# Performance work log

Measured on AMD Instinct MI355X. Metric: run time of the kernel, lower is better.

## Reference

```python
import math
import jax, jax.numpy as jnp
import numpy as np

EPS = 1e-5  # BatchNorm1d default eps


def setup_inputs() -> dict:
    key = jax.random.key(0)
    ks = jax.random.split(key, 8)
    B, H, N, L, CD = 16, 64, 64, 16384, 3
    dt_min, dt_max = 1e-3, 1e-1
    # DSSM parameters (as in __init__)
    log_dt = jax.random.uniform(ks[0], (H,)) * (math.log(dt_max) - math.log(dt_min)) + math.log(dt_min)
    C_ri = jax.random.normal(ks[1], (H, N, 2))  # view_as_real of complex C
    log_A_real = jnp.log(0.5 * jnp.ones((H, N)))
    A_imag = math.pi * jnp.tile(jnp.arange(N, dtype=jnp.float32)[None, :], (H, 1))
    D = jax.random.normal(ks[2], (H,))
    # FiLM adaptor: Linear(cond_dim, 2*H)
    film_w = jax.random.normal(ks[3], (2 * H, CD)) / np.sqrt(CD)
    film_b = jnp.zeros((2 * H,))
    u = jax.random.normal(ks[4], (B, H, L))
    cond = jax.random.uniform(ks[5], (B, CD))
    length = jax.random.randint(ks[6], (B,), 1, L + 1)
    return dict(u=u, cond=cond, length=length, log_dt=log_dt, C_ri=C_ri,
                log_A_real=log_A_real, A_imag=A_imag, D=D,
                film_w=film_w, film_b=film_b)


def _dssm(u, length, log_dt, C_ri, log_A_real, A_imag, D):
    # u: (B, H, L). Length-agnostic equivalent of the torch length-bucketed path:
    # mask input beyond each example's length (bucket slicing u[idxs,:,:l]),
    # do one full-length linear FFT conv, then zero output beyond the length
    # (out[idxs,:,:l] = y leaves the tail at zero).
    B, H, L = u.shape
    dt = jnp.exp(log_dt)                       # (H,)
    C = C_ri[..., 0] + 1j * C_ri[..., 1]       # (H, N) complex
    A = -jnp.exp(log_A_real) + 1j * A_imag     # (H, N) complex
    dtA = A * dt[:, None]                      # (H, N)
    t = jnp.arange(L, dtype=jnp.float32)
    P = jnp.exp(dtA[:, :, None] * t)           # (H, N, L) complex
    Ck = C * (jnp.exp(dtA) - 1.0) / A          # (H, N)
    K = 2.0 * jnp.einsum('hn,hnl->hl', Ck, P).real  # (H, L) real kernel
    mask = (t[None, :] < length[:, None]).astype(u.dtype)  # (B, L)
    um = u * mask[:, None, :]
    n = 2 * L  # rfft size; linear conv of length-L signals has length 2L-1 <= 2L
    y = jnp.fft.irfft(jnp.fft.rfft(um, n=n) * jnp.fft.rfft(K, n=n)[None], n=n)[..., :L]
    y = (y + um * D[:, None]) * mask[:, None, :]
    return y


def _film(y, cond, film_w, film_b):
    # BatchNorm1d(affine=False), training-mode batch stats over (B, L) per channel
    H = y.shape[1]
    gb = cond @ film_w.T + film_b               # (B, 2H)
    g, b = gb[:, :H, None], gb[:, H:, None]
    mean = y.mean(axis=(0, 2))
    var = y.var(axis=(0, 2))                    # biased variance (torch BN normalization)
    yn = (y - mean[None, :, None]) * jax.lax.rsqrt(var[None, :, None] + EPS)
    return yn * g + b


def reference(u, cond, length, log_dt, C_ri, log_A_real, A_imag, D, film_w, film_b):
    y = _dssm(u, length, log_dt, C_ri, log_A_real, A_imag, D)
    y = _film(y, cond, film_w, film_b)
    y = jnp.tanh(y)
    return u + y  # residual connection around the conditioned SSM block
```

## Files before the change

### kernel.cpp

```cpp
#include <hip/hip_runtime.h>
#include <hip/hip_bf16.h>

typedef __hip_bfloat16 bf16;
typedef __attribute__((ext_vector_type(8))) short s16x8;
typedef __attribute__((ext_vector_type(4))) float f32x4;

#define SWZ(c) ((((c) ^ ((c) >> 3)) & 7) << 4)

__device__ __forceinline__ unsigned short f2b(float x){
    __hip_bfloat16 h = __float2bfloat16(x);
    return __builtin_bit_cast(unsigned short, h);
}
__device__ __forceinline__ float b2f(unsigned short s){
    unsigned int u = (unsigned int)s << 16;
    return __builtin_bit_cast(float, u);
}

__global__ __launch_bounds__(256) void k0_setup(const float* __restrict__ log_dt,
        const float* __restrict__ C_ri, const float* __restrict__ log_A_real,
        const float* __restrict__ A_imag, const float* __restrict__ Dp,
        float* __restrict__ rLtab, float* __restrict__ rStab,
        short* __restrict__ Qh,
        short* __restrict__ Pmh, short* __restrict__ Pml,
        short* __restrict__ Klh, short* __restrict__ Kll)
{
    __shared__ float arr[64][65];
    __shared__ float a0[64];
    __shared__ float kd[64];
    int h = blockIdx.x;
    int tid = threadIdx.x;
    int n = tid & 63, g = tid >> 6;
    int hn = h * 64 + n;
    double dtd  = exp((double)log_dt[h]);
    float  Aref = -expf(log_A_real[hn]);
    double Ared = (double)Aref;
    double Aimd = (double)A_imag[hn];
    double adt  = Aimd * dtd;
    float  mdt  = (float)(Ared * dtd);
    auto cexp = [&](float e, float& re, float& im){
        double a = adt * (double)e;
        double k = floor(a * 0.15915494309189535);
        float ang = (float)(a - k * 6.283185307179586);
        float si, co;
        __sincosf(ang, &si, &co);
        float mag = expf(mdt * e);
        re = mag * co; im = mag * si;
    };
    float rre, rim; cexp(1.f, rre, rim);
    float Cre = C_ri[2 * hn], Cim = C_ri[2 * hn + 1];
    float emre = rre - 1.f, emim = rim;
    float inva2 = 1.f / (Aref * Aref + (float)(Aimd * Aimd));
    float qre_ = (emre * Aref + emim * (float)Aimd) * inva2;
    float qim_ = (emim * Aref - emre * (float)Aimd) * inva2;
    float ckre = Cre * qre_ - Cim * qim_;
    float ckim = Cre * qim_ + Cim * qre_;
    {
        short* q0 = Qh + (size_t)h * 8192 + (2 * n) * 64;
        short* q1 = q0 + 64;
        for (int t = 16 * g; t < 16 * g + 16; ++t) {
            float pre, pim; cexp((float)(63 - t), pre, pim);
            q0[t] = (short)f2b(pre);
            q1[t] = (short)f2b(pim);
        }
    }
    if (g == 0) {
        float pre, pim; cexp(64.f, pre, pim);
        rLtab[2 * hn] = pre; rLtab[2 * hn + 1] = pim;
    }
    if (g == 1) {
        float pre, pim; cexp(1024.f, pre, pim);
        rStab[2 * hn] = pre; rStab[2 * hn + 1] = pim;
    }
    if (g == 2) a0[n] = 2.f * ckre;
    {
        short* pmh = Pmh + (size_t)h * 8192;
        short* pml = Pml + (size_t)h * 8192;
        for (int j = 16 * g; j < 16 * g + 16; ++j) {
            float pre, pim; cexp((float)(j + 1), pre, pim);
            float wre = 2.f * (ckre * pre - ckim * pim);
            float wim = 2.f * (ckre * pim + ckim * pre);
            unsigned short h0 = f2b(wre), h1 = f2b(-wim);
            pmh[j * 128 + 2 * n]     = (short)h0;
            pml[j * 128 + 2 * n]     = (short)f2b(wre - b2f(h0));
            pmh[j * 128 + 2 * n + 1] = (short)h1;
            pml[j * 128 + 2 * n + 1] = (short)f2b(-wim - b2f(h1));
            arr[j][n] = wre;
        }
    }
    __syncthreads();
    if (tid < 64) {
        int d = tid;
        float s = 0.f;
        if (d == 0) { for (int k = 0; k < 64; ++k) s += a0[k]; }
        else        { for (int k = 0; k < 64; ++k) s += arr[d - 1][k]; }
        kd[d] = s;
    }
    __syncthreads();
    {
        float Dh = Dp[h];
        short* klh = Klh + (size_t)h * 4096 + n * 64;
        short* kll = Kll + (size_t)h * 4096 + n * 64;
        for (int t = 16 * g; t < 16 * g + 16; ++t) {
            if (t <= n) {
                float v = kd[n - t] + ((t == n) ? Dh : 0.f);
                unsigned short h0 = f2b(v);
                klh[t] = (short)h0;
                kll[t] = (short)f2b(v - b2f(h0));
            } else { klh[t] = 0; kll[t] = 0; }
        }
    }
}

__global__ __launch_bounds__(256, 2) void k_fused(const float* __restrict__ u,
        const int* __restrict__ length,
        const float* __restrict__ rLtab, const float* __restrict__ rStab,
        const short* __restrict__ Qh,
        const short* __restrict__ Pmh, const short* __restrict__ Pml,
        const short* __restrict__ Klh, const short* __restrict__ Kll,
        bf16* __restrict__ y, double* __restrict__ stats)
{
    __shared__ __align__(16) unsigned char lds[49152];
    unsigned char* carr = lds + 32768;
    int bh = blockIdx.x;
    int b = bh >> 6, h = bh & 63;
    int tid = threadIdx.x;
    int w = tid >> 6, lane = tid & 63;
    int lo = lane & 15, hi = lane >> 4;
    int len = length[b];
    const float* ub = u + (size_t)bh * 16384;

    s16x8 xh[4][2], xl[4][2];
    #pragma unroll
    for (int ct = 0; ct < 4; ++ct) {
        int c = w * 64 + ct * 16 + lo;
        #pragma unroll
        for (int kt = 0; kt < 2; ++kt) {
            int gidx = c * 64 + kt * 32 + hi * 8;
            float4 v0 = *(const float4*)(ub + gidx);
            float4 v1 = *(const float4*)(ub + gidx + 4);
            float xv[8] = {v0.x, v0.y, v0.z, v0.w, v1.x, v1.y, v1.z, v1.w};
            s16x8 fh, fl;
            #pragma unroll
            for (int e = 0; e < 8; ++e) {
                float xm = (gidx + e < len) ? xv[e] : 0.f;
                unsigned short h0 = f2b(xm);
                fh[e] = (short)h0;
                fl[e] = (short)f2b(xm - b2f(h0));
            }
            xh[ct][kt] = fh;
            xl[ct][kt] = fl;
        }
    }

    f32x4 acc[4][4];
    #pragma unroll
    for (int ct = 0; ct < 4; ++ct)
        #pragma unroll
        for (int jt = 0; jt < 4; ++jt)
            acc[ct][jt] = f32x4{0.f, 0.f, 0.f, 0.f};
    {
        const short* klhb = Klh + (size_t)h * 4096;
        const short* kllb = Kll + (size_t)h * 4096;
        #pragma unroll
        for (int kt = 0; kt < 2; ++kt) {
            #pragma unroll
            for (int jt = 0; jt < 4; ++jt) {
                s16x8 kfh = *(const s16x8*)(klhb + (jt * 16 + lo) * 64 + kt * 32 + hi * 8);
                s16x8 kfl = *(const s16x8*)(kllb + (jt * 16 + lo) * 64 + kt * 32 + hi * 8);
                #pragma unroll
                for (int ct = 0; ct < 4; ++ct) {
                    acc[ct][jt] = __builtin_amdgcn_mfma_f32_16x16x32_bf16(xh[ct][kt], kfh, acc[ct][jt], 0, 0, 0);
                    acc[ct][jt] = __builtin_amdgcn_mfma_f32_16x16x32_bf16(xh[ct][kt], kfl, acc[ct][jt], 0, 0, 0);
                    acc[ct][jt] = __builtin_amdgcn_mfma_f32_16x16x32_bf16(xl[ct][kt], kfh, acc[ct][jt], 0, 0, 0);
                }
            }
        }
    }

    auto gemm1 = [&](int q){
        const short* qb = Qh + (size_t)h * 8192 + (q * 32) * 64;
        #pragma unroll
        for (int mtq = 0; mtq < 2; ++mtq) {
            s16x8 q0 = *(const s16x8*)(qb + (mtq * 16 + lo) * 64 + hi * 8);
            s16x8 q1 = *(const s16x8*)(qb + (mtq * 16 + lo) * 64 + 32 + hi * 8);
            #pragma unroll
            for (int ct = 0; ct < 4; ++ct) {
                f32x4 sc = f32x4{0.f, 0.f, 0.f, 0.f};
                sc = __builtin_amdgcn_mfma_f32_16x16x32_bf16(q0, xh[ct][0], sc, 0, 0, 0);
                sc = __builtin_amdgcn_mfma_f32_16x16x32_bf16(q1, xh[ct][1], sc, 0, 0, 0);
                sc = __builtin_amdgcn_mfma_f32_16x16x32_bf16(q0, xl[ct][0], sc, 0, 0, 0);
                sc = __builtin_amdgcn_mfma_f32_16x16x32_bf16(q1, xl[ct][1], sc, 0, 0, 0);
                int c = w * 64 + ct * 16 + lo;
                *(f32x4*)(lds + c * 128 + ((mtq * 64 + hi * 16) ^ SWZ(c))) = sc;
            }
        }
    };

    gemm1(0);
    for (int q = 0; q < 4; ++q) {
        __syncthreads();
        {
            int m = tid >> 4, s = tid & 15;
            int gm = (h * 64 + q * 16 + m) * 2;
            float r64re = rLtab[gm], r64im = rLtab[gm + 1];
            float pre = rStab[gm],  pim = rStab[gm + 1];
            float ere = 0.f, eim = 0.f;
            #pragma unroll
            for (int i = 0; i < 16; ++i) {
                int c = 16 * s + i;
                float2 v = *(const float2*)(lds + c * 128 + ((8 * m) ^ SWZ(c)));
                float nre = fmaf(r64re, ere, fmaf(-r64im, eim, v.x));
                eim = fmaf(r64re, eim, fmaf(r64im, ere, v.y));
                ere = nre;
            }
            #pragma unroll
            for (int d = 1; d < 16; d <<= 1) {
                float orr = __shfl(ere, (lane - d) & 63, 64);
                float oii = __shfl(eim, (lane - d) & 63, 64);
                if (s >= d) {
                    float nre = fmaf(pre, orr, fmaf(-pim, oii, ere));
                    eim = fmaf(pre, oii, fmaf(pim, orr, eim));
                    ere = nre;
                }
                float t2 = pre * pre - pim * pim;
                pim = 2.f * pre * pim;
                pre = t2;
            }
            float cire = __shfl(ere, (lane - 1) & 63, 64);
            float ciim = __shfl(eim, (lane - 1) & 63, 64);
            if (s == 0) { cire = 0.f; ciim = 0.f; }
            int mh = m >> 2, ml = m & 3;
            #pragma unroll
            for (int i = 0; i < 16; ++i) {
                int c = 16 * s + i;
                float2 v = *(const float2*)(lds + c * 128 + ((8 * m) ^ SWZ(c)));
                int p16 = mh ^ (c & 3) ^ ((c >> 4) & 3);
                *(unsigned int*)(carr + c * 64 + 16 * p16 + 4 * ml) =
                    (unsigned)f2b(cire) | ((unsigned)f2b(ciim) << 16);
                float nre = fmaf(r64re, cire, fmaf(-r64im, ciim, v.x));
                ciim = fmaf(r64re, ciim, fmaf(r64im, cire, v.y));
                cire = nre;
            }
        }
        __syncthreads();
        {
            const short* pmhb = Pmh + (size_t)h * 8192 + q * 32;
            const short* pmlb = Pml + (size_t)h * 8192 + q * 32;
            s16x8 af[4];
            #pragma unroll
            for (int ct = 0; ct < 4; ++ct) {
                int c = w * 64 + ct * 16 + lo;
                int p16 = hi ^ (c & 3) ^ ((c >> 4) & 3);
                af[ct] = *(const s16x8*)(carr + c * 64 + 16 * p16);
            }
            #pragma unroll
            for (int jt = 0; jt < 4; ++jt) {
                s16x8 pfh = *(const s16x8*)(pmhb + (jt * 16 + lo) * 128 + hi * 8);
                s16x8 pfl = *(const s16x8*)(pmlb + (jt * 16 + lo) * 128 + hi * 8);
                #pragma unroll
                for (int ct = 0; ct < 4; ++ct) {
                    acc[ct][jt] = __builtin_amdgcn_mfma_f32_16x16x32_bf16(af[ct], pfh, acc[ct][jt], 0, 0, 0);
                    acc[ct][jt] = __builtin_amdgcn_mfma_f32_16x16x32_bf16(af[ct], pfl, acc[ct][jt], 0, 0, 0);
                }
            }
        }
        if (q < 3) gemm1(q + 1);
    }

    #pragma unroll
    for (int ct = 0; ct < 4; ++ct) {
        #pragma unroll
        for (int jt = 0; jt < 4; ++jt) {
            int j = jt * 16 + lo;
            #pragma unroll
            for (int rg = 0; rg < 4; ++rg) {
                int c = w * 64 + ct * 16 + hi * 4 + rg;
                *(unsigned short*)(lds + c * 128 + ((2 * j) ^ SWZ(c))) = f2b(acc[ct][jt][rg]);
            }
        }
    }
    __syncthreads();

    float s1 = 0.f, s2 = 0.f;
    short* yg = (short*)y + (size_t)bh * 16384;
    #pragma unroll
    for (int k = 0; k < 8; ++k) {
        int eidx = (k * 256 + tid) * 8;
        int row = eidx >> 6;
        int byt = ((eidx & 63) * 2) ^ SWZ(row);
        s16x8 yv = *(const s16x8*)(lds + row * 128 + byt);
        s16x8 o;
        #pragma unroll
        for (int e = 0; e < 8; ++e) {
            float vv = b2f((unsigned short)yv[e]);
            vv = (eidx + e < len) ? vv : 0.f;
            o[e] = (short)f2b(vv);
            s1 += vv;
            s2 = fmaf(vv, vv, s2);
        }
        *(s16x8*)(yg + eidx) = o;
    }
    #pragma unroll
    for (int off = 32; off > 0; off >>= 1) {
        s1 += __shfl_down(s1, off, 64);
        s2 += __shfl_down(s2, off, 64);
    }
    if (lane == 0) {
        atomicAdd(&stats[2 * h],     (double)s1);
        atomicAdd(&stats[2 * h + 1], (double)s2);
    }
}

__global__ __launch_bounds__(256) void k4_final(const float* __restrict__ u,
        const bf16* __restrict__ y, const float* __restrict__ cond,
        const float* __restrict__ fw, const float* __restrict__ fb,
        const double* __restrict__ stats, float* __restrict__ out)
{
    int tid = threadIdx.x;
    size_t idx8 = ((size_t)blockIdx.x * 256 + tid) * 8;
    int bh = (int)(idx8 >> 14);
    int b = bh >> 6, h = bh & 63;
    __shared__ float gg[2];
    if (tid == 0) {
        float g = fb[h], bb = fb[64 + h];
        #pragma unroll
        for (int k = 0; k < 3; ++k) {
            g  = fmaf(cond[b * 3 + k], fw[h * 3 + k], g);
            bb = fmaf(cond[b * 3 + k], fw[(64 + h) * 3 + k], bb);
        }
        gg[0] = g; gg[1] = bb;
    }
    __syncthreads();
    double inv = 1.0 / (16.0 * 16384.0);
    double mean_d = stats[2 * h] * inv;
    double var_d  = stats[2 * h + 1] * inv - mean_d * mean_d;
    float mean = (float)mean_d;
    float rstd = rsqrtf((float)var_d + 1e-5f);
    float gv = gg[0], bv = gg[1];
    float4 u0 = *(const float4*)(u + idx8);
    float4 u1 = *(const float4*)(u + idx8 + 4);
    s16x8 yv = *(const s16x8*)((const short*)y + idx8);
    float uv[8] = {u0.x, u0.y, u0.z, u0.w, u1.x, u1.y, u1.z, u1.w};
    float ov[8];
    #pragma unroll
    for (int e = 0; e < 8; ++e) {
        float z = fmaf((b2f((unsigned short)yv[e]) - mean) * rstd, gv, bv);
        ov[e] = uv[e] + tanhf(z);
    }
    *(float4*)(out + idx8)     = float4{ov[0], ov[1], ov[2], ov[3]};
    *(float4*)(out + idx8 + 4) = float4{ov[4], ov[5], ov[6], ov[7]};
}

extern "C" void kernel_launch(void* const* d_in, const int* in_sizes, int n_in,
                              void* d_out, int out_size, void* d_ws, size_t ws_size,
                              hipStream_t stream)
{
    const float* u           = (const float*)d_in[0];
    const float* cond        = (const float*)d_in[1];
    const int*   length      = (const int*)  d_in[2];
    const float* log_dt      = (const float*)d_in[3];
    const float* C_ri        = (const float*)d_in[4];
    const float* log_A_real  = (const float*)d_in[5];
    const float* A_imag      = (const float*)d_in[6];
    const float* D           = (const float*)d_in[7];
    const float* film_w      = (const float*)d_in[8];
    const float* film_b      = (const float*)d_in[9];
    float* out = (float*)d_out;

    char* w = (char*)d_ws;
    bf16*   y      = (bf16*)w;
    short*  Qh     = (short*)(w + 33554432);
    short*  Pmh    = (short*)(w + 34603008);
    short*  Pml    = (short*)(w + 35651584);
    short*  Klh    = (short*)(w + 36700160);
    short*  Kll    = (short*)(w + 37224448);
    float*  rLtab  = (float*)(w + 37748736);
    float*  rStab  = (float*)(w + 37781504);
    double* stats  = (double*)(w + 37814272);

    hipMemsetAsync(stats, 0, 1024, stream);
    hipLaunchKernelGGL(k0_setup, dim3(64),   dim3(256), 0, stream,
                       log_dt, C_ri, log_A_real, A_imag, D,
                       rLtab, rStab, Qh, Pmh, Pml, Klh, Kll);
    hipLaunchKernelGGL(k_fused,  dim3(1024), dim3(256), 0, stream,
                       u, length, rLtab, rStab, Qh, Pmh, Pml, Klh, Kll, y, stats);
    hipLaunchKernelGGL(k4_final, dim3(8192), dim3(256), 0, stream,
                       u, y, cond, film_w, film_b, stats, out);
}
```

Measured before the change: 114.4 us.

## Store chunk-state scratch as bf16 to halve LDS and raise occupancy

The per-chunk GEMM1 results are packed to bf16 pairs before going to shared memory instead of being stored as fp32, halving the scratch buffer from 32KB to 16KB. Total LDS drops from 48KB to 32KB per block, and launch bounds are raised to request 4 blocks per CU. Swizzle patterns are reworked for the new layout, and a barrier is added before the output staging because that region now overlaps the scratch. This trades precision in the intermediate recurrence inputs, and register pressure under the tighter launch bound, for more resident blocks to hide latency.

```diff
diff --git a/kernel.cpp b/kernel.cpp
--- a/kernel.cpp
+++ b/kernel.cpp
@@ -5,7 +5,9 @@
 typedef __attribute__((ext_vector_type(8))) short s16x8;
 typedef __attribute__((ext_vector_type(4))) float f32x4;
 
-#define SWZ(c) ((((c) ^ ((c) >> 3)) & 7) << 4)
+#define SWZY(c) ((((c) ^ ((c) >> 3) ^ ((c) >> 4)) & 7) << 4)
+#define SDW(row, m) ((row) * 64 + (((m) ^ ((((row) >> 4) & 7) << 1)) << 2))
+#define P16(c, g) (((g) ^ ((c) & 3) ^ (((c) >> 2) & 3) ^ (((c) >> 4) & 3)) & 3)
 
 __device__ __forceinline__ unsigned short f2b(float x){
     __hip_bfloat16 h = __float2bfloat16(x);
@@ -111,7 +113,7 @@
     }
 }
 
-__global__ __launch_bounds__(256, 2) void k_fused(const float* __restrict__ u,
+__global__ __launch_bounds__(256, 4) void k_fused(const float* __restrict__ u,
         const int* __restrict__ length,
         const float* __restrict__ rLtab, const float* __restrict__ rStab,
         const short* __restrict__ Qh,
@@ -119,8 +121,8 @@
         const short* __restrict__ Klh, const short* __restrict__ Kll,
         bf16* __restrict__ y, double* __restrict__ stats)
 {
-    __shared__ __align__(16) unsigned char lds[49152];
-    unsigned char* carr = lds + 32768;
+    __shared__ __align__(16) unsigned char lds[32768];
+    unsigned char* carr = lds + 16384;
     int bh = blockIdx.x;
     int b = bh >> 6, h = bh & 63;
     int tid = threadIdx.x;
@@ -191,7 +193,10 @@
                 sc = __builtin_amdgcn_mfma_f32_16x16x32_bf16(q0, xl[ct][0], sc, 0, 0, 0);
                 sc = __builtin_amdgcn_mfma_f32_16x16x32_bf16(q1, xl[ct][1], sc, 0, 0, 0);
                 int c = w * 64 + ct * 16 + lo;
-                *(f32x4*)(lds + c * 128 + ((mtq * 64 + hi * 16) ^ SWZ(c))) = sc;
+                unsigned int p0 = (unsigned)f2b(sc[0]) | ((unsigned)f2b(sc[1]) << 16);
+                unsigned int p1 = (unsigned)f2b(sc[2]) | ((unsigned)f2b(sc[3]) << 16);
+                unsigned long long pp = (unsigned long long)p0 | ((unsigned long long)p1 << 32);
+                *(unsigned long long*)(lds + SDW(c, mtq * 8 + 2 * hi)) = pp;
             }
         }
     };
@@ -208,9 +213,11 @@
             #pragma unroll
             for (int i = 0; i < 16; ++i) {
                 int c = 16 * s + i;
-                float2 v = *(const float2*)(lds + c * 128 + ((8 * m) ^ SWZ(c)));
-                float nre = fmaf(r64re, ere, fmaf(-r64im, eim, v.x));
-                eim = fmaf(r64re, eim, fmaf(r64im, ere, v.y));
+                unsigned int v = *(const unsigned int*)(lds + SDW(c, m));
+                float vre = b2f((unsigned short)v);
+                float vim = b2f((unsigned short)(v >> 16));
+                float nre = fmaf(r64re, ere, fmaf(-r64im, eim, vre));
+                eim = fmaf(r64re, eim, fmaf(r64im, ere, vim));
                 ere = nre;
             }
             #pragma unroll
@@ -233,12 +240,13 @@
             #pragma unroll
             for (int i = 0; i < 16; ++i) {
                 int c = 16 * s + i;
-                float2 v = *(const float2*)(lds + c * 128 + ((8 * m) ^ SWZ(c)));
-                int p16 = mh ^ (c & 3) ^ ((c >> 4) & 3);
-                *(unsigned int*)(carr + c * 64 + 16 * p16 + 4 * ml) =
+                unsigned int v = *(const unsigned int*)(lds + SDW(c, m));
+                float vre = b2f((unsigned short)v);
+                float vim = b2f((unsigned short)(v >> 16));
+                *(unsigned int*)(carr + c * 64 + 16 * P16(c, mh) + 4 * ml) =
                     (unsigned)f2b(cire) | ((unsigned)f2b(ciim) << 16);
-                float nre = fmaf(r64re, cire, fmaf(-r64im, ciim, v.x));
-                ciim = fmaf(r64re, ciim, fmaf(r64im, cire, v.y));
+                float nre = fmaf(r64re, cire, fmaf(-r64im, ciim, vre));
+                ciim = fmaf(r64re, ciim, fmaf(r64im, cire, vim));
                 cire = nre;
             }
         }
@@ -250,8 +258,7 @@
             #pragma unroll
             for (int ct = 0; ct < 4; ++ct) {
                 int c = w * 64 + ct * 16 + lo;
-                int p16 = hi ^ (c & 3) ^ ((c >> 4) & 3);
-                af[ct] = *(const s16x8*)(carr + c * 64 + 16 * p16);
+                af[ct] = *(const s16x8*)(carr + c * 64 + 16 * P16(c, hi));
             }
             #pragma unroll
             for (int jt = 0; jt < 4; ++jt) {
@@ -266,6 +273,7 @@
         }
         if (q < 3) gemm1(q + 1);
     }
+    __syncthreads();
 
     #pragma unroll
     for (int ct = 0; ct < 4; ++ct) {
@@ -275,7 +283,7 @@
             #pragma unroll
             for (int rg = 0; rg < 4; ++rg) {
                 int c = w * 64 + ct * 16 + hi * 4 + rg;
-                *(unsigned short*)(lds + c * 128 + ((2 * j) ^ SWZ(c))) = f2b(acc[ct][jt][rg]);
+                *(unsigned short*)(lds + c * 128 + ((2 * j) ^ SWZY(c))) = f2b(acc[ct][jt][rg]);
             }
         }
     }
@@ -287,7 +295,7 @@
     for (int k = 0; k < 8; ++k) {
         int eidx = (k * 256 + tid) * 8;
         int row = eidx >> 6;
-        int byt = ((eidx & 63) * 2) ^ SWZ(row);
+        int byt = ((eidx & 63) * 2) ^ SWZY(row);
         s16x8 yv = *(const s16x8*)(lds + row * 128 + byt);
         s16x8 o;
         #pragma unroll
```

Measured after the change: 196.7 us. 1.72x slower.
